# Performance work log

Hardware: AMD Instinct MI355X
Metric: run time of the kernel (lower is better)

## Reference

```python
import jax, jax.numpy as jnp
import numpy as np

B, T, F = 32, 2048, 512
H = 512          # hidden_dim
NC = 64          # num_classes
H4 = 4 * H       # concatenated i,f,g,o gates


def setup_inputs() -> dict:
    key = jax.random.key(0)
    ks = jax.random.split(key, 10)
    s = 0.02
    return {
        "features": jax.random.normal(ks[0], (B, T, F), jnp.float32),
        # layer 0: input dense (no bias) + hidden dense (bias), flax LSTMCell style
        "Wi0": jax.random.normal(ks[1], (F, H4), jnp.float32) * s,
        "Wh0": jax.random.normal(ks[2], (H, H4), jnp.float32) * s,
        "bh0": jnp.zeros((H4,), jnp.float32),
        # layer 1
        "Wi1": jax.random.normal(ks[3], (H, H4), jnp.float32) * s,
        "Wh1": jax.random.normal(ks[4], (H, H4), jnp.float32) * s,
        "bh1": jnp.zeros((H4,), jnp.float32),
        # output head
        "Wout": jax.random.normal(ks[5], (H, NC), jnp.float32) * s,
        "bout": jnp.zeros((NC,), jnp.float32),
    }


def _lstm_step(c, h, x, Wi, Wh, bh):
    # flax LSTMCell math with gates concatenated in (i, f, g, o) order
    z = x @ Wi + h @ Wh + bh          # [B, 4H]
    i, f, g, o = jnp.split(z, 4, axis=-1)
    i = jax.nn.sigmoid(i)
    f = jax.nn.sigmoid(f)
    g = jnp.tanh(g)
    o = jax.nn.sigmoid(o)
    c_new = f * c + i * g
    h_new = o * jnp.tanh(c_new)
    return c_new, h_new


def reference(features, Wi0, Wh0, bh0, Wi1, Wh1, bh1, Wout, bout):
    b = features.shape[0]
    z = jnp.zeros((b, H), features.dtype)
    init = (z, z, z, z)  # (c0, h0, c1, h1)

    def step(carry, x_t):
        c0, h0, c1, h1 = carry
        c0, h0 = _lstm_step(c0, h0, x_t, Wi0, Wh0, bh0)
        # dropout is deterministic (training=False) -> identity
        c1, h1 = _lstm_step(c1, h1, h0, Wi1, Wh1, bh1)
        return (c0, h0, c1, h1), None

    xs = jnp.swapaxes(features, 0, 1)  # [T, B, F]
    (c0, h0, c1, h1), _ = jax.lax.scan(step, init, xs)
    return h1 @ Wout + bout  # [B, num_classes]
```

## Files before the change

### kernel.cpp

```cpp
#include <hip/hip_runtime.h>
#include <math.h>

#define T_STEPS 2048
#define B_SZ 32
#define F_SZ 512
#define H_SZ 512
#define H4_SZ 2048
#define NC_SZ 64
#define NBLK 64
#define RINGE 16384
#define FLAG_STRIDE 32
#define REG_SZ 139264
#define XCD_AREA (4096 + 8 * REG_SZ)
#define R8_AREA 335872
#define COMBO_WS_NEED (XCD_AREA + R8_AREA)
#define POLL_CAP (1 << 14)

typedef _Float16 f16x8 __attribute__((ext_vector_type(8)));
typedef float f32x4 __attribute__((ext_vector_type(4)));

#define TIDX(l, w, rt, ct) (((((l)*4 + (w))*2 + (rt))*2 + (ct)))

#define ST16_SC0(p_, v_)                                                        \
    asm volatile("global_store_short %0, %1, off sc0"                           \
                 :: "v"(p_), "v"((unsigned)(v_)) : "memory")
#define ST32_SC0(p_, v_)                                                        \
    asm volatile("global_store_dword %0, %1, off sc0"                           \
                 :: "v"(p_), "v"((unsigned)(v_)) : "memory")

#define LDFRAG16_BODY(SC)                                                       \
    "global_load_dwordx4 %0, %16, off " SC "\n\t"                               \
    "global_load_dwordx4 %1, %16, off offset:1024 " SC "\n\t"                   \
    "global_load_dwordx4 %2, %16, off offset:2048 " SC "\n\t"                   \
    "global_load_dwordx4 %3, %16, off offset:3072 " SC "\n\t"                   \
    "global_load_dwordx4 %4, %17, off " SC "\n\t"                               \
    "global_load_dwordx4 %5, %17, off offset:1024 " SC "\n\t"                   \
    "global_load_dwordx4 %6, %17, off offset:2048 " SC "\n\t"                   \
    "global_load_dwordx4 %7, %17, off offset:3072 " SC "\n\t"                   \
    "global_load_dwordx4 %8, %18, off " SC "\n\t"                               \
    "global_load_dwordx4 %9, %18, off offset:1024 " SC "\n\t"                   \
    "global_load_dwordx4 %10, %18, off offset:2048 " SC "\n\t"                  \
    "global_load_dwordx4 %11, %18, off offset:3072 " SC "\n\t"                  \
    "global_load_dwordx4 %12, %19, off " SC "\n\t"                              \
    "global_load_dwordx4 %13, %19, off offset:1024 " SC "\n\t"                  \
    "global_load_dwordx4 %14, %19, off offset:2048 " SC "\n\t"                  \
    "global_load_dwordx4 %15, %19, off offset:3072 " SC "\n\t"                  \
    "s_waitcnt vmcnt(0)"

#define LDFRAG16_OUTS(d)                                                        \
    : "=&v"(d[0][0]), "=&v"(d[1][0]), "=&v"(d[0][1]), "=&v"(d[1][1]),           \
      "=&v"(d[0][2]), "=&v"(d[1][2]), "=&v"(d[0][3]), "=&v"(d[1][3]),           \
      "=&v"(d[0][4]), "=&v"(d[1][4]), "=&v"(d[0][5]), "=&v"(d[1][5]),           \
      "=&v"(d[0][6]), "=&v"(d[1][6]), "=&v"(d[0][7]), "=&v"(d[1][7])

#define LDFRAG16_CP(d, a0, a1, a2, a3)                                          \
  asm volatile(LDFRAG16_BODY("sc0 sc1") LDFRAG16_OUTS(d)                        \
    : "v"(a0), "v"(a1), "v"(a2), "v"(a3) : "memory")

#define LDFRAG16_L2(d, a0, a1, a2, a3)                                          \
  asm volatile(LDFRAG16_BODY("sc0") LDFRAG16_OUTS(d)                            \
    : "v"(a0), "v"(a1), "v"(a2), "v"(a3) : "memory")

#define PREFETCH_X(tt_) do {                                                         \
    if (wv < 2 && (tt_) < T_STEPS) {                                                 \
        _Pragma("unroll")                                                            \
        for (int rt = 0; rt < 2; ++rt) {                                             \
            const float* xr = feats                                                  \
                + ((size_t)(rt * 16 + rlane) * T_STEPS + (size_t)(tt_)) * F_SZ       \
                + 256 * wv + klo;                                                    \
            _Pragma("unroll")                                                        \
            for (int ks = 0; ks < 8; ++ks) {                                         \
                const float4 p0 = *(const float4*)(xr + 32 * ks);                    \
                const float4 p1 = *(const float4*)(xr + 32 * ks + 4);                \
                f16x8 t;                                                             \
                t[0] = (_Float16)p0.x; t[1] = (_Float16)p0.y;                        \
                t[2] = (_Float16)p0.z; t[3] = (_Float16)p0.w;                        \
                t[4] = (_Float16)p1.x; t[5] = (_Float16)p1.y;                        \
                t[6] = (_Float16)p1.z; t[7] = (_Float16)p1.w;                        \
                xf[rt][ks] = t;                                                      \
            }                                                                        \
        }                                                                            \
    }                                                                                \
} while (0)

#define LOAD_WEIGHTS()                                                               \
    _Pragma("unroll")                                                                \
    for (int ct = 0; ct < 2; ++ct) {                                                 \
        const int cc   = ct * 16 + rlane;                                            \
        const int jcol = (cc >> 3) * H_SZ + hbase + (cc & 7);                        \
        _Pragma("unroll")                                                            \
        for (int ks = 0; ks < 8; ++ks) {                                             \
            const int k0 = 256 * wv + 32 * ks + klo;                                 \
            f16x8 f0, f1;                                                            \
            _Pragma("unroll")                                                        \
            for (int i = 0; i < 8; ++i) {                                            \
                const int k = k0 + i;                                                \
                const float v0 = (k < H_SZ) ? Wi0[(size_t)k * H4_SZ + jcol]          \
                                : Wh0[(size_t)(k - H_SZ) * H4_SZ + jcol];            \
                const float v1 = (k < H_SZ) ? Wh1[(size_t)k * H4_SZ + jcol]          \
                                : Wi1[(size_t)(k - H_SZ) * H4_SZ + jcol];            \
                f0[i] = (_Float16)v0;                                                \
                f1[i] = (_Float16)v1;                                                \
            }                                                                        \
            wf0[ct][ks] = f0;                                                        \
            wf1[ct][ks] = f1;                                                        \
        }                                                                            \
    }

#define GATES(L, bias, creg, outstmt) do {                                           \
    float z[4];                                                                      \
    _Pragma("unroll")                                                                \
    for (int g = 0; g < 4; ++g) {                                                    \
        const int cc = g * 8 + gu, ct = cc >> 4, col = cc & 15;                      \
        float v = bias[g];                                                           \
        _Pragma("unroll")                                                            \
        for (int w = 0; w < 4; ++w)                                                  \
            v += zs[TIDX(L, w, grt, ct) * 272 + grow * 17 + col];                    \
        z[g] = v;                                                                    \
    }                                                                                \
    const float ig = 1.f / (1.f + expf(-z[0]));                                      \
    const float fg = 1.f / (1.f + expf(-z[1]));                                      \
    const float gg = tanhf(z[2]);                                                    \
    const float og = 1.f / (1.f + expf(-z[3]));                                      \
    creg = fg * creg + ig * gg;                                                      \
    const float hv = og * tanhf(creg);                                               \
    outstmt;                                                                         \
} while (0)

#define MFMA_QUAD(arr0, arr1, wf)                                                    \
    f32x4 a00 = {0,0,0,0}, a01 = {0,0,0,0}, a10 = {0,0,0,0}, a11 = {0,0,0,0};        \
    _Pragma("unroll")                                                                \
    for (int ks = 0; ks < 8; ++ks) {                                                 \
        a00 = __builtin_amdgcn_mfma_f32_16x16x32_f16(arr0, wf[0][ks], a00, 0, 0, 0); \
        a01 = __builtin_amdgcn_mfma_f32_16x16x32_f16(arr0, wf[1][ks], a01, 0, 0, 0); \
        a10 = __builtin_amdgcn_mfma_f32_16x16x32_f16(arr1, wf[0][ks], a10, 0, 0, 0); \
        a11 = __builtin_amdgcn_mfma_f32_16x16x32_f16(arr1, wf[1][ks], a11, 0, 0, 0); \
    }

#define ZS_STORE(L)                                                                  \
    _Pragma("unroll")                                                                \
    for (int q = 0; q < 4; ++q) {                                                    \
        zs[TIDX(L, wv, 0, 0) * 272 + (r0 + q) * 17 + ccl] = a00[q];                  \
        zs[TIDX(L, wv, 0, 1) * 272 + (r0 + q) * 17 + ccl] = a01[q];                  \
        zs[TIDX(L, wv, 1, 0) * 272 + (r0 + q) * 17 + ccl] = a10[q];                  \
        zs[TIDX(L, wv, 1, 1) * 272 + (r0 + q) * 17 + ccl] = a11[q];                  \
    }

__global__ __launch_bounds__(256, 2) void lstm_xcd(
    const float* __restrict__ feats,
    const float* __restrict__ Wi0, const float* __restrict__ Wh0,
    const float* __restrict__ bh0,
    const float* __restrict__ Wi1, const float* __restrict__ Wh1,
    const float* __restrict__ bh1,
    const float* __restrict__ Wout, const float* __restrict__ bout,
    float* __restrict__ out,
    char* __restrict__ wsbase)
{
    const int tid   = threadIdx.x;
    const int lane  = tid & 63;
    const int wv    = tid >> 6;
    const int rlane = lane & 15;
    const int klo   = (lane >> 4) * 8;

    __shared__ float zs[32 * 272];
    __shared__ float ps[256];
    __shared__ unsigned role_s;
    __shared__ int dead_s;

    unsigned xcc;
    asm volatile("s_getreg_b32 %0, hwreg(HW_REG_XCC_ID)" : "=s"(xcc));
    xcc &= 7;
    unsigned* ctr     = (unsigned*)(wsbase + (size_t)xcc * 128);
    unsigned* alldone = (unsigned*)(wsbase + 1024);
    unsigned* success = (unsigned*)(wsbase + 1152);
    if (tid == 0) {
        role_s = __hip_atomic_fetch_add(ctr, 1u, __ATOMIC_RELAXED,
                                        __HIP_MEMORY_SCOPE_AGENT);
        dead_s = 0;
    }
    __syncthreads();
    const unsigned role = role_s;
    if (role >= 64) return;
    const int jb    = (int)role;
    const int hbase = jb * 8;

    char* regn = wsbase + 4096 + (size_t)xcc * REG_SZ;
    _Float16* h0ring = (_Float16*)regn;
    _Float16* h1ring = (_Float16*)(regn + 65536);
    unsigned* flags  = (unsigned*)(regn + 131072);

    f16x8 wf0[2][8], wf1[2][8];
    LOAD_WEIGHTS();

    const int gb = tid >> 3, gu = tid & 7;
    const int grow = gb & 15, grt = gb >> 4;
    float c0 = 0.f, c1 = 0.f;
    float bias0[4], bias1[4];
    #pragma unroll
    for (int g = 0; g < 4; ++g) {
        bias0[g] = bh0[g * H_SZ + hbase + gu];
        bias1[g] = bh1[g * H_SZ + hbase + gu];
    }
    const int eidx = (jb >> 5) * 8192
                   + ((((jb >> 2) & 7) * 2) + (gb >> 4)) * 512
                   + ((jb & 3) * 16 + (gb & 15)) * 8 + gu;

    f16x8 xf[2][8];
    PREFETCH_X(0);

#define POLL_XCD(val_) do {                                                          \
    if (tid < 64) {                                                                  \
        const unsigned* fp_ = flags + (size_t)lane * FLAG_STRIDE;                    \
        unsigned f_; int spins_ = 0;                                                 \
        for (;;) {                                                                   \
            asm volatile("global_load_dword %0, %1, off sc0\n\t"                     \
                         "s_waitcnt vmcnt(0)"                                        \
                         : "=&v"(f_) : "v"(fp_) : "memory");                         \
            if (f_ >= (unsigned)(val_)) break;                                       \
            if ((++spins_ & 63) == 0) {                                              \
                unsigned ad_;                                                        \
                asm volatile("global_load_dword %0, %1, off sc0 sc1\n\t"             \
                             "s_waitcnt vmcnt(0)"                                    \
                             : "=&v"(ad_) : "v"(alldone) : "memory");                \
                if (ad_ || spins_ > POLL_CAP) { dead_s = 1; break; }                 \
            }                                                                        \
        }                                                                            \
    }                                                                                \
    __syncthreads();                                                                 \
    if (dead_s) return;                                                              \
} while (0)

    for (int it = 0; it <= T_STEPS; ++it) {
        POLL_XCD(it);

        f16x8 hA[2][8];
        if (wv >= 2) {
            const _Float16* b = h0ring + (size_t)((it + 1) & 1) * RINGE
                                + (wv - 2) * 8192 + lane * 8;
            LDFRAG16_L2(hA, b, b + 2048, b + 4096, b + 6144);
        } else if (it > 0) {
            const _Float16* b = h1ring + (size_t)(it & 1) * RINGE
                                + wv * 8192 + lane * 8;
            LDFRAG16_L2(hA, b, b + 2048, b + 4096, b + 6144);
        }

        const int r0 = (lane >> 4) * 4, ccl = lane & 15;

        if (it < T_STEPS) {
            if (wv < 2) { MFMA_QUAD(xf[0][ks], xf[1][ks], wf0); ZS_STORE(0); }
            else        { MFMA_QUAD(hA[0][ks], hA[1][ks], wf0); ZS_STORE(0); }
        }
        if (it > 0) {
            MFMA_QUAD(hA[0][ks], hA[1][ks], wf1); ZS_STORE(1);
        }
        __syncthreads();

        if (it < T_STEPS) {
            GATES(0, bias0, c0, {
                union { _Float16 h; unsigned short s; } cv; cv.h = (_Float16)hv;
                _Float16* p = h0ring + (size_t)(it & 1) * RINGE + eidx;
                ST16_SC0(p, cv.s);
            });
        }
        if (it > 0) {
            GATES(1, bias1, c1, {
                union { _Float16 h; unsigned short s; } cv; cv.h = (_Float16)hv;
                _Float16* p = h1ring + (size_t)((it + 1) & 1) * RINGE + eidx;
                ST16_SC0(p, cv.s);
            });
        }
        asm volatile("s_waitcnt vmcnt(0)" ::: "memory");
        __syncthreads();
        if (tid == 0)
            ST32_SC0(flags + (size_t)jb * FLAG_STRIDE, (unsigned)(it + 1));

        PREFETCH_X(it + 1);
    }

    POLL_XCD(T_STEPS + 1);

    {
        const _Float16* hf = h1ring + (size_t)((T_STEPS + 1) & 1) * RINGE;
        const int b = tid & 31, kc = tid >> 5;
        float part = 0.f;
        #pragma unroll
        for (int o = 0; o < 8; ++o) {
            const int k0 = kc * 64 + o * 8;
            const int idx = (k0 >> 8) * 8192
                          + (((k0 >> 5) & 7) * 2 + (b >> 4)) * 512
                          + (((k0 >> 3) & 3) * 16 + (b & 15)) * 8;
            f16x8 hv8;
            asm volatile("global_load_dwordx4 %0, %1, off sc0\n\t"
                         "s_waitcnt vmcnt(0)"
                         : "=&v"(hv8) : "v"(hf + idx) : "memory");
            #pragma unroll
            for (int j = 0; j < 8; ++j)
                part += (float)hv8[j] * Wout[(size_t)(k0 + j) * NC_SZ + jb];
        }
        ps[kc * 32 + b] = part;
        __syncthreads();
        if (tid < 32) {
            float acc = bout[jb];
            #pragma unroll
            for (int c = 0; c < 8; ++c) acc += ps[c * 32 + tid];
            out[tid * NC_SZ + jb] = acc;
        }
    }
    asm volatile("s_waitcnt vmcnt(0)" ::: "memory");
    __syncthreads();
    if (tid == 0) {
        __hip_atomic_store(success, 1u, __ATOMIC_RELAXED, __HIP_MEMORY_SCOPE_AGENT);
        __hip_atomic_store(alldone, 1u, __ATOMIC_RELAXED, __HIP_MEMORY_SCOPE_AGENT);
    }
#undef POLL_XCD
}

__global__ __launch_bounds__(256, 1) void lstm_persistent(
    const float* __restrict__ feats,
    const float* __restrict__ Wi0, const float* __restrict__ Wh0,
    const float* __restrict__ bh0,
    const float* __restrict__ Wi1, const float* __restrict__ Wh1,
    const float* __restrict__ bh1,
    const float* __restrict__ Wout, const float* __restrict__ bout,
    float* __restrict__ out,
    _Float16* __restrict__ h0ring, _Float16* __restrict__ h1ring,
    float* __restrict__ h1fin, unsigned* __restrict__ flags,
    const unsigned* __restrict__ success)
{
    if (__hip_atomic_load(success, __ATOMIC_RELAXED, __HIP_MEMORY_SCOPE_AGENT))
        return;

    const int tid   = threadIdx.x;
    const int lane  = tid & 63;
    const int wv    = tid >> 6;
    const int jb    = blockIdx.x;
    const int hbase = jb * 8;
    const int rlane = lane & 15;
    const int klo   = (lane >> 4) * 8;

    __shared__ float zs[32 * 272];
    __shared__ float ps[256];

    f16x8 wf0[2][8], wf1[2][8];
    LOAD_WEIGHTS();

    const int gb = tid >> 3, gu = tid & 7;
    const int grow = gb & 15, grt = gb >> 4;
    float c0 = 0.f, c1 = 0.f;
    float bias0[4], bias1[4];
    #pragma unroll
    for (int g = 0; g < 4; ++g) {
        bias0[g] = bh0[g * H_SZ + hbase + gu];
        bias1[g] = bh1[g * H_SZ + hbase + gu];
    }
    const int eidx = (jb >> 5) * 8192
                   + ((((jb >> 2) & 7) * 2) + (gb >> 4)) * 512
                   + ((jb & 3) * 16 + (gb & 15)) * 8 + gu;

    f16x8 xf[2][8];
    PREFETCH_X(0);

    for (int it = 0; it <= T_STEPS; ++it) {
        if (tid < 64) {
            while (__hip_atomic_load(&flags[(size_t)lane * FLAG_STRIDE],
                                     __ATOMIC_RELAXED, __HIP_MEMORY_SCOPE_AGENT)
                   < (unsigned)it) { }
        }
        __syncthreads();

        f16x8 hA[2][8];
        if (wv >= 2) {
            const _Float16* b = h0ring + (size_t)((it + 1) & 1) * RINGE
                                + (wv - 2) * 8192 + lane * 8;
            LDFRAG16_CP(hA, b, b + 2048, b + 4096, b + 6144);
        } else if (it > 0) {
            const _Float16* b = h1ring + (size_t)(it & 1) * RINGE
                                + wv * 8192 + lane * 8;
            LDFRAG16_CP(hA, b, b + 2048, b + 4096, b + 6144);
        }

        const int r0 = (lane >> 4) * 4, ccl = lane & 15;

        if (it < T_STEPS) {
            if (wv < 2) { MFMA_QUAD(xf[0][ks], xf[1][ks], wf0); ZS_STORE(0); }
            else        { MFMA_QUAD(hA[0][ks], hA[1][ks], wf0); ZS_STORE(0); }
        }
        if (it > 0) {
            MFMA_QUAD(hA[0][ks], hA[1][ks], wf1); ZS_STORE(1);
        }
        __syncthreads();

        if (it < T_STEPS) {
            GATES(0, bias0, c0, {
                union { _Float16 h; unsigned short s; } cv; cv.h = (_Float16)hv;
                __hip_atomic_store(
                    (unsigned short*)(h0ring + (size_t)(it & 1) * RINGE + eidx),
                    cv.s, __ATOMIC_RELAXED, __HIP_MEMORY_SCOPE_AGENT);
            });
        }
        if (it > 0) {
            GATES(1, bias1, c1, {
                union { _Float16 h; unsigned short s; } cv; cv.h = (_Float16)hv;
                __hip_atomic_store(
                    (unsigned short*)(h1ring + (size_t)((it + 1) & 1) * RINGE + eidx),
                    cv.s, __ATOMIC_RELAXED, __HIP_MEMORY_SCOPE_AGENT);
                if (it == T_STEPS) {
                    union { float f; unsigned u; } cf; cf.f = hv;
                    __hip_atomic_store((unsigned*)(h1fin + gb * H_SZ + hbase + gu),
                                       cf.u, __ATOMIC_RELAXED,
                                       __HIP_MEMORY_SCOPE_AGENT);
                }
            });
        }
        asm volatile("s_waitcnt vmcnt(0)" ::: "memory");
        __syncthreads();
        if (tid == 0)
            __hip_atomic_store(&flags[(size_t)jb * FLAG_STRIDE], (unsigned)(it + 1),
                               __ATOMIC_RELAXED, __HIP_MEMORY_SCOPE_AGENT);

        PREFETCH_X(it + 1);
    }

    if (tid < 64) {
        while (__hip_atomic_load(&flags[(size_t)lane * FLAG_STRIDE],
                                 __ATOMIC_RELAXED, __HIP_MEMORY_SCOPE_AGENT)
               < (unsigned)(T_STEPS + 1)) { }
    }
    __syncthreads();

    {
        const int b = tid & 31, kc = tid >> 5;
        float part = 0.f;
        for (int k = kc * 64; k < kc * 64 + 64; ++k) {
            union { unsigned u; float f; } cv;
            cv.u = __hip_atomic_load((const unsigned*)(h1fin + b * H_SZ + k),
                                     __ATOMIC_RELAXED, __HIP_MEMORY_SCOPE_AGENT);
            part += cv.f * Wout[(size_t)k * NC_SZ + jb];
        }
        ps[kc * 32 + b] = part;
        __syncthreads();
        if (tid < 32) {
            float acc = bout[jb];
            #pragma unroll
            for (int c = 0; c < 8; ++c) acc += ps[c * 32 + tid];
            out[tid * NC_SZ + jb] = acc;
        }
    }
}

extern "C" void kernel_launch(void* const* d_in, const int* in_sizes, int n_in,
                              void* d_out, int out_size, void* d_ws, size_t ws_size,
                              hipStream_t stream) {
    const float* feats = (const float*)d_in[0];
    const float* Wi0   = (const float*)d_in[1];
    const float* Wh0   = (const float*)d_in[2];
    const float* bh0   = (const float*)d_in[3];
    const float* Wi1   = (const float*)d_in[4];
    const float* Wh1   = (const float*)d_in[5];
    const float* bh1   = (const float*)d_in[6];
    const float* Wout  = (const float*)d_in[7];
    const float* bout  = (const float*)d_in[8];

    if (ws_size >= (size_t)COMBO_WS_NEED) {
        hipMemsetAsync(d_ws, 0, COMBO_WS_NEED, stream);
        char* ws = (char*)d_ws;
        char* r8 = ws + XCD_AREA;
        lstm_xcd<<<dim3(512), dim3(256), 0, stream>>>(
            feats, Wi0, Wh0, bh0, Wi1, Wh1, bh1, Wout, bout,
            (float*)d_out, ws);
        lstm_persistent<<<dim3(NBLK), dim3(256), 0, stream>>>(
            feats, Wi0, Wh0, bh0, Wi1, Wh1, bh1, Wout, bout,
            (float*)d_out,
            (_Float16*)(r8), (_Float16*)(r8 + 131072),
            (float*)(r8 + 262144), (unsigned*)(r8 + 327680),
            (const unsigned*)(ws + 1152));
    } else {
        char* ws = (char*)d_ws;
        hipMemsetAsync(d_ws, 0, R8_AREA + 128, stream);
        lstm_persistent<<<dim3(NBLK), dim3(256), 0, stream>>>(
            feats, Wi0, Wh0, bh0, Wi1, Wh1, bh1, Wout, bout,
            (float*)d_out,
            (_Float16*)(ws), (_Float16*)(ws + 131072),
            (float*)(ws + 262144), (unsigned*)(ws + 327680),
            (const unsigned*)(ws + R8_AREA));
    }
}
```

Before: 18.47 ms.

## Split per-step barrier into separate layer-0 and layer-1 flag arrays

Replaces the single per-step flag array with two, flags0 for the layer-0 h ring and flags1 for the layer-1 h ring. Layer 1's h1-dependent part now waits only on flags1, after layer-0 gates are published, and waves poll individually rather than one wave gating the block. The intent is to loosen the lockstep wavefront so layer-0 progress is not held up by layer-1 completion, shortening the serial critical path per step. In exchange each step does two flag publish/poll rounds with extra block barriers, and the workspace region per XCD grows to hold the second flag array.

```diff
diff --git a/kernel.cpp b/kernel.cpp
--- a/kernel.cpp
+++ b/kernel.cpp
@@ -10,7 +10,7 @@
 #define NBLK 64
 #define RINGE 16384
 #define FLAG_STRIDE 32
-#define REG_SZ 139264
+#define REG_SZ 147456
 #define XCD_AREA (4096 + 8 * REG_SZ)
 #define R8_AREA 335872
 #define COMBO_WS_NEED (XCD_AREA + R8_AREA)
@@ -187,7 +187,8 @@
     char* regn = wsbase + 4096 + (size_t)xcc * REG_SZ;
     _Float16* h0ring = (_Float16*)regn;
     _Float16* h1ring = (_Float16*)(regn + 65536);
-    unsigned* flags  = (unsigned*)(regn + 131072);
+    unsigned* flags0 = (unsigned*)(regn + 131072);
+    unsigned* flags1 = (unsigned*)(regn + 139264);
 
     f16x8 wf0[2][8], wf1[2][8];
     LOAD_WEIGHTS();
@@ -208,53 +209,40 @@
     f16x8 xf[2][8];
     PREFETCH_X(0);
 
-#define POLL_XCD(val_) do {                                                          \
-    if (tid < 64) {                                                                  \
-        const unsigned* fp_ = flags + (size_t)lane * FLAG_STRIDE;                    \
-        unsigned f_; int spins_ = 0;                                                 \
-        for (;;) {                                                                   \
-            asm volatile("global_load_dword %0, %1, off sc0\n\t"                     \
+#define POLL_WAVE(farr_, val_) do {                                                  \
+    const unsigned* fp_ = (farr_) + (size_t)lane * FLAG_STRIDE;                      \
+    unsigned f_; int spins_ = 0;                                                     \
+    for (;;) {                                                                       \
+        asm volatile("global_load_dword %0, %1, off sc0\n\t"                         \
+                     "s_waitcnt vmcnt(0)"                                            \
+                     : "=&v"(f_) : "v"(fp_) : "memory");                             \
+        if (f_ >= (unsigned)(val_)) break;                                           \
+        if ((++spins_ & 63) == 0) {                                                  \
+            unsigned ad_;                                                            \
+            asm volatile("global_load_dword %0, %1, off sc0 sc1\n\t"                 \
                          "s_waitcnt vmcnt(0)"                                        \
-                         : "=&v"(f_) : "v"(fp_) : "memory");                         \
-            if (f_ >= (unsigned)(val_)) break;                                       \
-            if ((++spins_ & 63) == 0) {                                              \
-                unsigned ad_;                                                        \
-                asm volatile("global_load_dword %0, %1, off sc0 sc1\n\t"             \
-                             "s_waitcnt vmcnt(0)"                                    \
-                             : "=&v"(ad_) : "v"(alldone) : "memory");                \
-                if (ad_ || spins_ > POLL_CAP) { dead_s = 1; break; }                 \
-            }                                                                        \
+                         : "=&v"(ad_) : "v"(alldone) : "memory");                    \
+            if (ad_ || spins_ > POLL_CAP) { dead_s = 1; break; }                     \
         }                                                                            \
     }                                                                                \
-    __syncthreads();                                                                 \
-    if (dead_s) return;                                                              \
 } while (0)
 
     for (int it = 0; it <= T_STEPS; ++it) {
-        POLL_XCD(it);
-
         f16x8 hA[2][8];
+
         if (wv >= 2) {
+            POLL_WAVE(flags0, it);
             const _Float16* b = h0ring + (size_t)((it + 1) & 1) * RINGE
                                 + (wv - 2) * 8192 + lane * 8;
             LDFRAG16_L2(hA, b, b + 2048, b + 4096, b + 6144);
-        } else if (it > 0) {
-            const _Float16* b = h1ring + (size_t)(it & 1) * RINGE
-                                + wv * 8192 + lane * 8;
-            LDFRAG16_L2(hA, b, b + 2048, b + 4096, b + 6144);
-        }
-
+        }
         const int r0 = (lane >> 4) * 4, ccl = lane & 15;
-
         if (it < T_STEPS) {
             if (wv < 2) { MFMA_QUAD(xf[0][ks], xf[1][ks], wf0); ZS_STORE(0); }
             else        { MFMA_QUAD(hA[0][ks], hA[1][ks], wf0); ZS_STORE(0); }
         }
-        if (it > 0) {
-            MFMA_QUAD(hA[0][ks], hA[1][ks], wf1); ZS_STORE(1);
-        }
-        __syncthreads();
-
+        __syncthreads();
+        if (dead_s) return;
         if (it < T_STEPS) {
             GATES(0, bias0, c0, {
                 union { _Float16 h; unsigned short s; } cv; cv.h = (_Float16)hv;
@@ -262,6 +250,22 @@
                 ST16_SC0(p, cv.s);
             });
         }
+        asm volatile("s_waitcnt vmcnt(0)" ::: "memory");
+        __syncthreads();
+        if (tid == 0)
+            ST32_SC0(flags0 + (size_t)jb * FLAG_STRIDE, (unsigned)(it + 1));
+
+        if (wv < 2 && it > 0) {
+            POLL_WAVE(flags1, it);
+            const _Float16* b = h1ring + (size_t)(it & 1) * RINGE
+                                + wv * 8192 + lane * 8;
+            LDFRAG16_L2(hA, b, b + 2048, b + 4096, b + 6144);
+        }
+        if (it > 0) {
+            MFMA_QUAD(hA[0][ks], hA[1][ks], wf1); ZS_STORE(1);
+        }
+        __syncthreads();
+        if (dead_s) return;
         if (it > 0) {
             GATES(1, bias1, c1, {
                 union { _Float16 h; unsigned short s; } cv; cv.h = (_Float16)hv;
@@ -272,12 +276,14 @@
         asm volatile("s_waitcnt vmcnt(0)" ::: "memory");
         __syncthreads();
         if (tid == 0)
-            ST32_SC0(flags + (size_t)jb * FLAG_STRIDE, (unsigned)(it + 1));
+            ST32_SC0(flags1 + (size_t)jb * FLAG_STRIDE, (unsigned)(it + 1));
 
         PREFETCH_X(it + 1);
     }
 
-    POLL_XCD(T_STEPS + 1);
+    if (tid < 64) POLL_WAVE(flags1, T_STEPS + 1);
+    __syncthreads();
+    if (dead_s) return;
 
     {
         const _Float16* hf = h1ring + (size_t)((T_STEPS + 1) & 1) * RINGE;
@@ -312,7 +318,7 @@
         __hip_atomic_store(success, 1u, __ATOMIC_RELAXED, __HIP_MEMORY_SCOPE_AGENT);
         __hip_atomic_store(alldone, 1u, __ATOMIC_RELAXED, __HIP_MEMORY_SCOPE_AGENT);
     }
-#undef POLL_XCD
+#undef POLL_WAVE
 }
 
 __global__ __launch_bounds__(256, 1) void lstm_persistent(
```

After: 23.73 ms. 1.28x slower.
